# Kernel optimization log

Measured on AMD Instinct MI355X. Metric: run time of the kernel, lower is better.

The kernel has to match this reference:

```python
import jax, jax.numpy as jnp
import numpy as np

B, T, A_DIM, Z_DIM, K = 128, 80, 32, 64, 16


def setup_inputs() -> dict:
    key = jax.random.key(0)
    k1, k2, k3, k4 = jax.random.split(key, 4)
    obs = jax.random.normal(k1, (B, T, A_DIM), jnp.float32)
    alpha_logits = jax.random.normal(k2, (B, T, K), jnp.float32)
    # torch init: A = eye(z) repeated K times; small noise keeps 80-step recursion stable
    A_K = jnp.eye(Z_DIM, dtype=jnp.float32)[None] + 0.005 * jax.random.normal(k3, (K, Z_DIM, Z_DIM), jnp.float32)
    # torch init: C = 0.05 * randn
    C_K = 0.05 * jax.random.normal(k4, (K, A_DIM, Z_DIM), jnp.float32)
    return {"obs": obs, "alpha_logits": alpha_logits, "A_K": A_K, "C_K": C_K}


def _kalman(obs, A, C):
    # obs [B,T,a], A [B,T,z,z], C [B,T,a,z]
    Bq, Tq, a_dim = obs.shape
    z_dim = A.shape[-1]
    dt = obs.dtype
    Q = 0.08 * jnp.eye(z_dim, dtype=dt)
    R = 0.03 * jnp.eye(a_dim, dtype=dt)
    I = jnp.eye(z_dim, dtype=dt)

    obs_t = jnp.swapaxes(obs, 0, 1)          # [T,B,a]
    A_t = jnp.swapaxes(A, 0, 1)              # [T,B,z,z]
    C_t = jnp.swapaxes(C, 0, 1)              # [T,B,a,z]
    A_next = jnp.concatenate([A_t[1:], A_t[-1:]], axis=0)  # A[t+1]; last unused

    mu0 = jnp.zeros((Bq, z_dim), dt)
    sig0 = jnp.broadcast_to(20.0 * I, (Bq, z_dim, z_dim))

    def filt_step(carry, inp):
        mu_p, sig_p, mu_prev = carry
        At, Anx, Ct, y = inp
        CtT = jnp.swapaxes(Ct, -1, -2)
        S = Ct @ sig_p @ CtT + R                       # [B,a,a]
        Kg = sig_p @ CtT @ jnp.linalg.inv(S)            # [B,z,a]
        Amu = jnp.einsum('bij,bj->bi', At, mu_prev)     # A_t mu_{t-1}
        err = y - jnp.einsum('bij,bj->bi', Ct, Amu)
        mu_f = Amu + jnp.einsum('bij,bj->bi', Kg, err)
        sig_f = (I - Kg @ Ct) @ sig_p
        mu_pn = jnp.einsum('bij,bj->bi', Anx, mu_f)     # prediction with A_{t+1}
        sig_pn = Anx @ sig_f @ jnp.swapaxes(Anx, -1, -2) + Q
        return (mu_pn, sig_pn, mu_f), (mu_f, sig_f, mu_p, sig_p)

    _, (mu_f, sig_f, mu_p, sig_p) = jax.lax.scan(
        filt_step, (mu0, sig0, mu0), (A_t, A_next, C_t, obs_t))

    def smooth_step(carry, inp):
        mu_s, sig_s = carry
        mf, sf, Anx, mpn, spn = inp
        J = sf @ jnp.swapaxes(Anx, -1, -2) @ jnp.linalg.inv(spn)
        mu = mf + jnp.einsum('bij,bj->bi', J, mu_s - mpn)
        sig = sf + J @ (sig_s - spn) @ jnp.swapaxes(J, -1, -2)
        return (mu, sig), (mu, sig)

    init = (mu_f[-1], sig_f[-1])
    _, (mu_sm, sig_sm) = jax.lax.scan(
        smooth_step, init,
        (mu_f[:-1], sig_f[:-1], A_t[1:], mu_p[1:], sig_p[1:]),
        reverse=True)
    mu_sm = jnp.concatenate([mu_sm, mu_f[-1:]], axis=0)
    sig_sm = jnp.concatenate([sig_sm, sig_f[-1:]], axis=0)
    return jnp.swapaxes(mu_sm, 0, 1), jnp.swapaxes(sig_sm, 0, 1)  # [B,T,z], [B,T,z,z]


def reference(obs, alpha_logits, A_K, C_K):
    w = jax.nn.softmax(alpha_logits, axis=-1)                # [B,T,K]
    A = jnp.einsum('btk,kij->btij', w, A_K)                  # [B,T,z,z]
    C = jnp.einsum('btk,kij->btij', w, C_K)                  # [B,T,a,z]
    return _kalman(obs, A, C)
```

## Files before the change

### kernel.cpp

```cpp
#include <hip/hip_runtime.h>

#define B_ 128
#define T_ 80
#define AD 32
#define ZD 64
#define KD 16
#define S8 68
#define S4 34

template<int KL, int AS, int BS, bool ATRANS>
__device__ __forceinline__ void mm64(const float* __restrict__ Pa, const float* __restrict__ Qb,
                                     float acc[2][4], int r2, int c4)
{
#pragma unroll 8
    for (int k = 0; k < KL; k++) {
        float aA, aB;
        if (ATRANS) { aA = Pa[k * AS + r2];   aB = Pa[k * AS + r2 + 1]; }
        else        { aA = Pa[r2 * AS + k];   aB = Pa[(r2 + 1) * AS + k]; }
        const float4 bv = *(const float4*)&Qb[k * BS + c4];
        acc[0][0] += aA * bv.x; acc[0][1] += aA * bv.y; acc[0][2] += aA * bv.z; acc[0][3] += aA * bv.w;
        acc[1][0] += aB * bv.x; acc[1][1] += aB * bv.y; acc[1][2] += aB * bv.z; acc[1][3] += aB * bv.w;
    }
}

__global__ __launch_bounds__(512, 2)
void kvae_kernel(const float* __restrict__ obs, const float* __restrict__ logits,
                 const float* __restrict__ AK, const float* __restrict__ CK,
                 float* __restrict__ out)
{
    __shared__ __align__(16) float W[T_ * KD];
    __shared__ __align__(16) float Am[ZD * S8];
    __shared__ __align__(16) float At[ZD * S8];
    __shared__ __align__(16) float SP[ZD * S8];
    __shared__ __align__(16) float SF[ZD * S8];
    __shared__ __align__(16) float Mm[ZD * S8];
    __shared__ __align__(16) float Pool[9792];
    __shared__ __align__(16) float y_s[32];
    __shared__ __align__(16) float mup[64];
    __shared__ __align__(16) float muf[64];
    __shared__ __align__(16) float mus[64];
    __shared__ __align__(16) float mpn[64];
    __shared__ __align__(16) float dv[64];

    float* T1 = Pool;
    float* CM = Pool + 2176;
    float* CT = Pool + 4352;
    float* U_ = Pool + 6528;
    float* S_ = Pool + 8704;
    float* Xb = Pool;
    float* SG = Pool + 4352;

    const int tid = threadIdx.x;
    const int b   = blockIdx.x;

    const int r16 = tid >> 4;
    const int cg  = tid & 15;
    const int c4  = cg << 2;
    const int c2  = cg << 1;
    const int r2  = r16 << 1;
    const int i64 = tid >> 3;
    const int c8  = (tid & 7) << 3;

    const float* obs_b = obs    + (size_t)b * T_ * AD;
    const float* lg_b  = logits + (size_t)b * T_ * KD;
    float* omu = out + (size_t)b * T_ * ZD;
    float* osg = out + (size_t)B_ * T_ * ZD + (size_t)b * T_ * ZD * ZD;
    const float4* AK4 = (const float4*)AK;
    const float4* CK4 = (const float4*)CK;

    auto mixA_full = [&](int tt) {
#pragma unroll
        for (int rr = 0; rr < 2; rr++) {
            int r = r2 + rr;
            float4 a = make_float4(0.f, 0.f, 0.f, 0.f);
#pragma unroll
            for (int k = 0; k < KD; k++) {
                float wk = W[tt * KD + k];
                float4 v = AK4[k * 1024 + r * 16 + cg];
                a.x += wk * v.x; a.y += wk * v.y; a.z += wk * v.z; a.w += wk * v.w;
            }
            *(float4*)&Am[r * S8 + c4] = a;
            At[(c4 + 0) * S8 + r] = a.x; At[(c4 + 1) * S8 + r] = a.y;
            At[(c4 + 2) * S8 + r] = a.z; At[(c4 + 3) * S8 + r] = a.w;
        }
    };
    auto mixC_full = [&](int tt) {
        float4 a = make_float4(0.f, 0.f, 0.f, 0.f);
#pragma unroll
        for (int k = 0; k < KD; k++) {
            float wk = W[tt * KD + k];
            float4 v = CK4[k * 512 + r16 * 16 + cg];
            a.x += wk * v.x; a.y += wk * v.y; a.z += wk * v.z; a.w += wk * v.w;
        }
        *(float4*)&CM[r16 * S8 + c4] = a;
        CT[(c4 + 0) * S4 + r16] = a.x; CT[(c4 + 1) * S4 + r16] = a.y;
        CT[(c4 + 2) * S4 + r16] = a.z; CT[(c4 + 3) * S4 + r16] = a.w;
    };

    if (tid < T_) {
        float l[KD]; float mx = -1e30f;
#pragma unroll
        for (int k = 0; k < KD; k++) { l[k] = lg_b[tid * KD + k]; mx = fmaxf(mx, l[k]); }
        float s = 0.f;
#pragma unroll
        for (int k = 0; k < KD; k++) { l[k] = expf(l[k] - mx); s += l[k]; }
        float inv = 1.0f / s;
#pragma unroll
        for (int k = 0; k < KD; k++) W[tid * KD + k] = l[k] * inv;
    }
#pragma unroll
    for (int rr = 0; rr < 2; rr++) {
        int r = r2 + rr;
#pragma unroll
        for (int j = 0; j < 4; j++) SP[r * S8 + c4 + j] = (r == c4 + j) ? 20.0f : 0.0f;
    }
    if (tid < ZD) mup[tid] = 0.0f;
    __syncthreads();

    for (int t = 0; t < T_; t++) {
        if (t < T_ - 1) mixA_full(t + 1);
        mixC_full(t);
        if (tid < AD) y_s[tid] = obs_b[t * AD + tid];
        __syncthreads();

        {
            float a0 = 0, a1 = 0, a2 = 0, a3 = 0;
            const float* pa = CM + r16 * S8;
#pragma unroll 8
            for (int k = 0; k < ZD; k++) {
                float a = pa[k];
                float4 bv = *(const float4*)&SP[k * S8 + c4];
                a0 += a * bv.x; a1 += a * bv.y; a2 += a * bv.z; a3 += a * bv.w;
            }
            T1[r16 * S8 + c4 + 0] = a0; T1[r16 * S8 + c4 + 1] = a1;
            T1[r16 * S8 + c4 + 2] = a2; T1[r16 * S8 + c4 + 3] = a3;
        }
        __syncthreads();

        float4 ur; float ue = 0.f;
        {
            float a0 = 0, a1 = 0;
            const float* pa = T1 + r16 * S8;
#pragma unroll 8
            for (int k = 0; k < ZD; k++) {
                float a = pa[k];
                float2 bv = *(const float2*)&CT[k * S4 + c2];
                a0 += a * bv.x; a1 += a * bv.y;
            }
            if (r16 == c2)     a0 += 0.03f;
            if (r16 == c2 + 1) a1 += 0.03f;
            S_[r16 * S4 + c2] = a0; S_[r16 * S4 + c2 + 1] = a1;
            ur = *(const float4*)&T1[r16 * S8 + c4];
            if (cg == 15) {
                float s = 0.f;
                const float* pc = CM + r16 * S8;
#pragma unroll 8
                for (int k = 0; k < ZD; k++) s += pc[k] * mup[k];
                ue = y_s[r16] - s;
            }
            if (r16 < 2) {
                *(float4*)&U_[r16 * S8 + c4] = ur;
                if (cg == 15) U_[r16 * S8 + 64] = ue;
            }
        }
        __syncthreads();

#pragma unroll 1
        for (int j = 0; j < 16; j++) {
            const int p0 = 2 * j, p1 = p0 + 1;
            const int i = r16;
            const float f0 = S_[i * S4 + p0], f1 = S_[i * S4 + p1];
            const float qa = S_[p0 * S4 + p0], qb = S_[p0 * S4 + p1];
            const float qc = S_[p1 * S4 + p0], qd = S_[p1 * S4 + p1];
            const float l0x = S_[p0 * S4 + c2], l0y = S_[p0 * S4 + c2 + 1];
            const float l1x = S_[p1 * S4 + c2], l1y = S_[p1 * S4 + c2 + 1];
            const float4 r0 = *(const float4*)&U_[p0 * S8 + c4];
            const float4 r1 = *(const float4*)&U_[p1 * S8 + c4];
            float e0 = 0.f, e1 = 0.f;
            if (cg == 15) { e0 = U_[p0 * S8 + 64]; e1 = U_[p1 * S8 + 64]; }
            __syncthreads();
            const float dinv = 1.0f / (qa * qd - qb * qc);
            const float i00 =  qd * dinv, i01 = -qb * dinv;
            const float i10 = -qc * dinv, i11 =  qa * dinv;
            const float n0x = i00 * l0x + i01 * l1x, n0y = i00 * l0y + i01 * l1y;
            const float n1x = i10 * l0x + i11 * l1x, n1y = i10 * l0y + i11 * l1y;
            float4 m0, m1;
            m0.x = i00 * r0.x + i01 * r1.x; m0.y = i00 * r0.y + i01 * r1.y;
            m0.z = i00 * r0.z + i01 * r1.z; m0.w = i00 * r0.w + i01 * r1.w;
            m1.x = i10 * r0.x + i11 * r1.x; m1.y = i10 * r0.y + i11 * r1.y;
            m1.z = i10 * r0.z + i11 * r1.z; m1.w = i10 * r0.w + i11 * r1.w;
            const float me0 = i00 * e0 + i01 * e1, me1 = i10 * e0 + i11 * e1;
            if (i == p0) {
                S_[i * S4 + c2] = n0x; S_[i * S4 + c2 + 1] = n0y;
                ur = m0; if (cg == 15) ue = me0;
            } else if (i == p1) {
                S_[i * S4 + c2] = n1x; S_[i * S4 + c2 + 1] = n1y;
                ur = m1; if (cg == 15) ue = me1;
            } else {
                S_[i * S4 + c2]     -= f0 * n0x + f1 * n1x;
                S_[i * S4 + c2 + 1] -= f0 * n0y + f1 * n1y;
                ur.x -= f0 * m0.x + f1 * m1.x; ur.y -= f0 * m0.y + f1 * m1.y;
                ur.z -= f0 * m0.z + f1 * m1.z; ur.w -= f0 * m0.w + f1 * m1.w;
                if (cg == 15) ue -= f0 * me0 + f1 * me1;
            }
            if (j < 15 && (i == p0 + 2 || i == p0 + 3)) {
                *(float4*)&U_[i * S8 + c4] = ur;
                if (cg == 15) U_[i * S8 + 64] = ue;
            }
            __syncthreads();
        }
        *(float4*)&U_[r16 * S8 + c4] = ur;
        if (cg == 15) U_[r16 * S8 + 64] = ue;
        __syncthreads();

        {
            float acc[2][4] = {};
            mm64<AD, S8, S8, true>(T1, U_, acc, r2, c4);
            float* og = osg + (size_t)t * ZD * ZD;
#pragma unroll
            for (int rr = 0; rr < 2; rr++) {
                int r = r2 + rr;
                float4 sp = *(const float4*)&SP[r * S8 + c4];
                float4 v;
                v.x = sp.x - acc[rr][0]; v.y = sp.y - acc[rr][1];
                v.z = sp.z - acc[rr][2]; v.w = sp.w - acc[rr][3];
                *(float4*)&SF[r * S8 + c4] = v;
                *(float4*)(og + r * ZD + c4) = v;
            }
        }
        if (tid < ZD) {
            float s = 0.f;
#pragma unroll
            for (int k = 0; k < AD; k++) s += T1[k * S8 + tid] * U_[k * S8 + 64];
            float v = mup[tid] + s;
            muf[tid] = v;
            omu[t * ZD + tid] = v;
        }
        __syncthreads();

        if (t < T_ - 1) {
            {
                float acc[2][4] = {};
                mm64<ZD, S8, S8, false>(Am, SF, acc, r2, c4);
#pragma unroll
                for (int rr = 0; rr < 2; rr++)
                    *(float4*)&Mm[(r2 + rr) * S8 + c4] =
                        make_float4(acc[rr][0], acc[rr][1], acc[rr][2], acc[rr][3]);
            }
            __syncthreads();
            {
                float acc[2][4] = {};
                mm64<ZD, S8, S8, false>(Mm, At, acc, r2, c4);
#pragma unroll
                for (int rr = 0; rr < 2; rr++) {
                    int r = r2 + rr;
#pragma unroll
                    for (int j = 0; j < 4; j++)
                        SP[r * S8 + c4 + j] = acc[rr][j] + ((r == c4 + j) ? 0.08f : 0.0f);
                }
            }
            if (tid >= 448) {
                int i = tid - 448;
                float s = 0.f;
                const float* pa = Am + i * S8;
#pragma unroll 8
                for (int k = 0; k < ZD; k++) s += pa[k] * muf[k];
                mup[i] = s;
            }
            __syncthreads();
        }
    }

#pragma unroll
    for (int rr = 0; rr < 2; rr++) {
        int r = r2 + rr;
        *(float4*)&SG[r * S8 + c4] = *(const float4*)&SF[r * S8 + c4];
    }
    if (tid < ZD) mus[tid] = muf[tid];
    __syncthreads();

    for (int t = T_ - 2; t >= 0; t--) {
        mixA_full(t + 1);
        {
            const float4* og4 = (const float4*)(osg + (size_t)t * ZD * ZD);
#pragma unroll
            for (int rr = 0; rr < 2; rr++) {
                int r = r2 + rr;
                *(float4*)&SF[r * S8 + c4] = og4[r * 16 + cg];
            }
        }
        if (tid >= 448) muf[tid - 448] = omu[t * ZD + (tid - 448)];
        __syncthreads();

        {
            float acc[2][4] = {};
            mm64<ZD, S8, S8, false>(Am, SF, acc, r2, c4);
#pragma unroll
            for (int rr = 0; rr < 2; rr++) {
                int r = r2 + rr;
                float4 v = make_float4(acc[rr][0], acc[rr][1], acc[rr][2], acc[rr][3]);
                *(float4*)&Mm[r * S8 + c4] = v;
                *(float4*)&Xb[r * S8 + c4] = v;
            }
        }
        if (tid >= 448) {
            int i = tid - 448;
            float s = 0.f;
            const float* pa = Am + i * S8;
#pragma unroll 8
            for (int k = 0; k < ZD; k++) s += pa[k] * muf[k];
            mpn[i] = s;
        }
        __syncthreads();

        {
            float acc[2][4] = {};
            mm64<ZD, S8, S8, false>(Mm, At, acc, r2, c4);
#pragma unroll
            for (int rr = 0; rr < 2; rr++) {
                int r = r2 + rr;
#pragma unroll
                for (int j = 0; j < 4; j++)
                    SP[r * S8 + c4 + j] = acc[rr][j] + ((r == c4 + j) ? 0.08f : 0.0f);
            }
        }
        if (tid >= 448) { int i = tid - 448; dv[i] = mus[i] - mpn[i]; }
        __syncthreads();

        float4 xr0 = *(const float4*)&Xb[i64 * S8 + c8];
        float4 xr1 = *(const float4*)&Xb[i64 * S8 + c8 + 4];
#pragma unroll 1
        for (int j = 0; j < 32; j++) {
            const int p0 = 2 * j, p1 = p0 + 1;
            const float f0 = SP[i64 * S8 + p0], f1 = SP[i64 * S8 + p1];
            const float qa = SP[p0 * S8 + p0], qb = SP[p0 * S8 + p1];
            const float qc = SP[p1 * S8 + p0], qd = SP[p1 * S8 + p1];
            const float4 l0a = *(const float4*)&SP[p0 * S8 + c8];
            const float4 l0b = *(const float4*)&SP[p0 * S8 + c8 + 4];
            const float4 l1a = *(const float4*)&SP[p1 * S8 + c8];
            const float4 l1b = *(const float4*)&SP[p1 * S8 + c8 + 4];
            const float4 r0a = *(const float4*)&Xb[p0 * S8 + c8];
            const float4 r0b = *(const float4*)&Xb[p0 * S8 + c8 + 4];
            const float4 r1a = *(const float4*)&Xb[p1 * S8 + c8];
            const float4 r1b = *(const float4*)&Xb[p1 * S8 + c8 + 4];
            const float4 ol0 = *(const float4*)&SP[i64 * S8 + c8];
            const float4 ol1 = *(const float4*)&SP[i64 * S8 + c8 + 4];
            __syncthreads();
            const float dinv = 1.0f / (qa * qd - qb * qc);
            const float i00 =  qd * dinv, i01 = -qb * dinv;
            const float i10 = -qc * dinv, i11 =  qa * dinv;
            float4 nl0a, nl0b, nl1a, nl1b, nr0a, nr0b, nr1a, nr1b;
            nl0a.x = i00*l0a.x + i01*l1a.x; nl0a.y = i00*l0a.y + i01*l1a.y;
            nl0a.z = i00*l0a.z + i01*l1a.z; nl0a.w = i00*l0a.w + i01*l1a.w;
            nl0b.x = i00*l0b.x + i01*l1b.x; nl0b.y = i00*l0b.y + i01*l1b.y;
            nl0b.z = i00*l0b.z + i01*l1b.z; nl0b.w = i00*l0b.w + i01*l1b.w;
            nl1a.x = i10*l0a.x + i11*l1a.x; nl1a.y = i10*l0a.y + i11*l1a.y;
            nl1a.z = i10*l0a.z + i11*l1a.z; nl1a.w = i10*l0a.w + i11*l1a.w;
            nl1b.x = i10*l0b.x + i11*l1b.x; nl1b.y = i10*l0b.y + i11*l1b.y;
            nl1b.z = i10*l0b.z + i11*l1b.z; nl1b.w = i10*l0b.w + i11*l1b.w;
            nr0a.x = i00*r0a.x + i01*r1a.x; nr0a.y = i00*r0a.y + i01*r1a.y;
            nr0a.z = i00*r0a.z + i01*r1a.z; nr0a.w = i00*r0a.w + i01*r1a.w;
            nr0b.x = i00*r0b.x + i01*r1b.x; nr0b.y = i00*r0b.y + i01*r1b.y;
            nr0b.z = i00*r0b.z + i01*r1b.z; nr0b.w = i00*r0b.w + i01*r1b.w;
            nr1a.x = i10*r0a.x + i11*r1a.x; nr1a.y = i10*r0a.y + i11*r1a.y;
            nr1a.z = i10*r0a.z + i11*r1a.z; nr1a.w = i10*r0a.w + i11*r1a.w;
            nr1b.x = i10*r0b.x + i11*r1b.x; nr1b.y = i10*r0b.y + i11*r1b.y;
            nr1b.z = i10*r0b.z + i11*r1b.z; nr1b.w = i10*r0b.w + i11*r1b.w;
            if (i64 == p0) {
                *(float4*)&SP[i64 * S8 + c8]     = nl0a;
                *(float4*)&SP[i64 * S8 + c8 + 4] = nl0b;
                xr0 = nr0a; xr1 = nr0b;
            } else if (i64 == p1) {
                *(float4*)&SP[i64 * S8 + c8]     = nl1a;
                *(float4*)&SP[i64 * S8 + c8 + 4] = nl1b;
                xr0 = nr1a; xr1 = nr1b;
            } else {
                float4 w0 = ol0, w1 = ol1;
                w0.x -= f0*nl0a.x + f1*nl1a.x; w0.y -= f0*nl0a.y + f1*nl1a.y;
                w0.z -= f0*nl0a.z + f1*nl1a.z; w0.w -= f0*nl0a.w + f1*nl1a.w;
                w1.x -= f0*nl0b.x + f1*nl1b.x; w1.y -= f0*nl0b.y + f1*nl1b.y;
                w1.z -= f0*nl0b.z + f1*nl1b.z; w1.w -= f0*nl0b.w + f1*nl1b.w;
                *(float4*)&SP[i64 * S8 + c8]     = w0;
                *(float4*)&SP[i64 * S8 + c8 + 4] = w1;
                xr0.x -= f0*nr0a.x + f1*nr1a.x; xr0.y -= f0*nr0a.y + f1*nr1a.y;
                xr0.z -= f0*nr0a.z + f1*nr1a.z; xr0.w -= f0*nr0a.w + f1*nr1a.w;
                xr1.x -= f0*nr0b.x + f1*nr1b.x; xr1.y -= f0*nr0b.y + f1*nr1b.y;
                xr1.z -= f0*nr0b.z + f1*nr1b.z; xr1.w -= f0*nr0b.w + f1*nr1b.w;
            }
            if (j < 31 && (i64 == p0 + 2 || i64 == p0 + 3)) {
                *(float4*)&Xb[i64 * S8 + c8]     = xr0;
                *(float4*)&Xb[i64 * S8 + c8 + 4] = xr1;
            }
            __syncthreads();
        }
        *(float4*)&Xb[i64 * S8 + c8]     = xr0;
        *(float4*)&Xb[i64 * S8 + c8 + 4] = xr1;
        __syncthreads();

        {
            float acc[2][4] = {};
            mm64<ZD, S8, S8, false>(SG, Xb, acc, r2, c4);
#pragma unroll
            for (int rr = 0; rr < 2; rr++) {
                int r = r2 + rr;
                float4 m = *(const float4*)&Mm[r * S8 + c4];
                SP[r * S8 + c4 + 0] = acc[rr][0] - m.x;
                SP[r * S8 + c4 + 1] = acc[rr][1] - m.y;
                SP[r * S8 + c4 + 2] = acc[rr][2] - m.z;
                SP[r * S8 + c4 + 3] = acc[rr][3] - m.w;
            }
        }
        __syncthreads();

        {
            float acc[2][4] = {};
            mm64<ZD, S8, S8, true>(Xb, SP, acc, r2, c4);
            float* og = osg + (size_t)t * ZD * ZD;
#pragma unroll
            for (int rr = 0; rr < 2; rr++) {
                int r = r2 + rr;
                float4 sf = *(const float4*)&SF[r * S8 + c4];
                float4 v;
                v.x = sf.x + acc[rr][0]; v.y = sf.y + acc[rr][1];
                v.z = sf.z + acc[rr][2]; v.w = sf.w + acc[rr][3];
                *(float4*)&SG[r * S8 + c4] = v;
                *(float4*)(og + r * ZD + c4) = v;
            }
        }
        if (tid < ZD) {
            float s = 0.f;
#pragma unroll 8
            for (int k = 0; k < ZD; k++) s += Xb[k * S8 + tid] * dv[k];
            float v = muf[tid] + s;
            mus[tid] = v;
            omu[t * ZD + tid] = v;
        }
        __syncthreads();
    }
}

extern "C" void kernel_launch(void* const* d_in, const int* in_sizes, int n_in,
                              void* d_out, int out_size, void* d_ws, size_t ws_size,
                              hipStream_t stream) {
    const float* obs = (const float*)d_in[0];
    const float* lg  = (const float*)d_in[1];
    const float* AK  = (const float*)d_in[2];
    const float* CK  = (const float*)d_in[3];
    (void)d_ws; (void)ws_size; (void)in_sizes; (void)n_in; (void)out_size;
    kvae_kernel<<<dim3(B_), dim3(512), 0, stream>>>(obs, lg, AK, CK, (float*)d_out);
}
```

Baseline: 3.979 ms.

## Rewrite Kalman kernel with 256 threads, 4x4 register tiles and pivot-broadcast elimination

Halves the block to 256 threads and gives each thread a 4x4 output tile in the 64x64 matrix products, with both operands read as float4. The Gauss-Jordan solves keep their rows in registers and publish only the next pivot rows and factors into double-buffered shared arrays, so the per-step serial solve work and shared traffic shrink. The symmetric predicted covariance is built for the upper triangle only and then mirrored. The cost is more registers per thread and a larger, more intricate kernel that is harder to check.

```diff
diff --git a/kernel.cpp b/kernel.cpp
--- a/kernel.cpp
+++ b/kernel.cpp
@@ -5,37 +5,54 @@
 #define AD 32
 #define ZD 64
 #define KD 16
-#define S8 68
-#define S4 34
-
-template<int KL, int AS, int BS, bool ATRANS>
-__device__ __forceinline__ void mm64(const float* __restrict__ Pa, const float* __restrict__ Qb,
-                                     float acc[2][4], int r2, int c4)
+#define SZ 68
+#define SC 36
+
+__device__ __forceinline__ float4 ld4(const float* p) { return *(const float4*)p; }
+__device__ __forceinline__ void st4f(float* p, float4 v) { *(float4*)p = v; }
+__device__ __forceinline__ float4 comb2(float a, float4 x, float b, float4 y) {
+    return make_float4(a*x.x + b*y.x, a*x.y + b*y.y, a*x.z + b*y.z, a*x.w + b*y.w);
+}
+__device__ __forceinline__ float4 elim2(float4 c, float g0, float4 x, float g1, float4 y) {
+    c.x -= g0*x.x + g1*y.x; c.y -= g0*x.y + g1*y.y;
+    c.z -= g0*x.z + g1*y.z; c.w -= g0*x.w + g1*y.w;
+    return c;
+}
+
+template<int KL, int AS, int BS>
+__device__ __forceinline__ void mmT44(const float* __restrict__ PaT, const float* __restrict__ Qb,
+                                      float acc[4][4], int r4, int c4)
 {
 #pragma unroll 8
-    for (int k = 0; k < KL; k++) {
-        float aA, aB;
-        if (ATRANS) { aA = Pa[k * AS + r2];   aB = Pa[k * AS + r2 + 1]; }
-        else        { aA = Pa[r2 * AS + k];   aB = Pa[(r2 + 1) * AS + k]; }
-        const float4 bv = *(const float4*)&Qb[k * BS + c4];
-        acc[0][0] += aA * bv.x; acc[0][1] += aA * bv.y; acc[0][2] += aA * bv.z; acc[0][3] += aA * bv.w;
-        acc[1][0] += aB * bv.x; acc[1][1] += aB * bv.y; acc[1][2] += aB * bv.z; acc[1][3] += aB * bv.w;
+    for (int k = 0; k < KL; ++k) {
+        const float4 av = ld4(&PaT[k*AS + r4]);
+        const float4 bv = ld4(&Qb[k*BS + c4]);
+        acc[0][0] += av.x*bv.x; acc[0][1] += av.x*bv.y; acc[0][2] += av.x*bv.z; acc[0][3] += av.x*bv.w;
+        acc[1][0] += av.y*bv.x; acc[1][1] += av.y*bv.y; acc[1][2] += av.y*bv.z; acc[1][3] += av.y*bv.w;
+        acc[2][0] += av.z*bv.x; acc[2][1] += av.z*bv.y; acc[2][2] += av.z*bv.z; acc[2][3] += av.z*bv.w;
+        acc[3][0] += av.w*bv.x; acc[3][1] += av.w*bv.y; acc[3][2] += av.w*bv.z; acc[3][3] += av.w*bv.w;
     }
 }
 
-__global__ __launch_bounds__(512, 2)
+__global__ __launch_bounds__(256, 1)
 void kvae_kernel(const float* __restrict__ obs, const float* __restrict__ logits,
                  const float* __restrict__ AK, const float* __restrict__ CK,
                  float* __restrict__ out)
 {
     __shared__ __align__(16) float W[T_ * KD];
-    __shared__ __align__(16) float Am[ZD * S8];
-    __shared__ __align__(16) float At[ZD * S8];
-    __shared__ __align__(16) float SP[ZD * S8];
-    __shared__ __align__(16) float SF[ZD * S8];
-    __shared__ __align__(16) float Mm[ZD * S8];
-    __shared__ __align__(16) float Pool[9792];
+    __shared__ __align__(16) float Am[ZD * SZ];
+    __shared__ __align__(16) float At[ZD * SZ];
+    __shared__ __align__(16) float SP[ZD * SZ];
+    __shared__ __align__(16) float SF[ZD * SZ];
+    __shared__ __align__(16) float MT[ZD * SZ];
+    __shared__ __align__(16) float Pool[9984];
+    __shared__ __align__(16) float pvL[256];
+    __shared__ __align__(16) float pvR[256];
+    __shared__ __align__(16) float fb[256];
+    __shared__ __align__(16) float pvE[4];
     __shared__ __align__(16) float y_s[32];
+    __shared__ __align__(16) float errv[32];
+    __shared__ __align__(16) float uev[32];
     __shared__ __align__(16) float mup[64];
     __shared__ __align__(16) float muf[64];
     __shared__ __align__(16) float mus[64];
@@ -45,21 +62,22 @@
     float* T1 = Pool;
     float* CM = Pool + 2176;
     float* CT = Pool + 4352;
-    float* U_ = Pool + 6528;
-    float* S_ = Pool + 8704;
-    float* Xb = Pool;
-    float* SG = Pool + 4352;
+    float* S_ = Pool + 6656;
+    float* U_ = Pool + 7808;
+    float* SG = Pool;
+    float* Xb = Pool + 4352;
 
     const int tid = threadIdx.x;
     const int b   = blockIdx.x;
-
-    const int r16 = tid >> 4;
     const int cg  = tid & 15;
     const int c4  = cg << 2;
+    const int r4  = (tid >> 4) << 2;
+    const int r2  = (tid >> 4) << 1;
     const int c2  = cg << 1;
-    const int r2  = r16 << 1;
-    const int i64 = tid >> 3;
-    const int c8  = (tid & 7) << 3;
+    const int gi  = tid >> 2;
+    const int gs  = tid & 3;
+    const int hi  = tid >> 3;
+    const int hs  = tid & 7;
 
     const float* obs_b = obs    + (size_t)b * T_ * AD;
     const float* lg_b  = logits + (size_t)b * T_ * KD;
@@ -68,33 +86,37 @@
     const float4* AK4 = (const float4*)AK;
     const float4* CK4 = (const float4*)CK;
 
-    auto mixA_full = [&](int tt) {
-#pragma unroll
-        for (int rr = 0; rr < 2; rr++) {
-            int r = r2 + rr;
+    auto mixA = [&](int tt) {
+#pragma unroll
+        for (int q = 0; q < 4; q++) {
+            const int r = r4 + q;
             float4 a = make_float4(0.f, 0.f, 0.f, 0.f);
 #pragma unroll
             for (int k = 0; k < KD; k++) {
-                float wk = W[tt * KD + k];
-                float4 v = AK4[k * 1024 + r * 16 + cg];
+                const float wk = W[tt * KD + k];
+                const float4 v = AK4[k * 1024 + r * 16 + cg];
                 a.x += wk * v.x; a.y += wk * v.y; a.z += wk * v.z; a.w += wk * v.w;
             }
-            *(float4*)&Am[r * S8 + c4] = a;
-            At[(c4 + 0) * S8 + r] = a.x; At[(c4 + 1) * S8 + r] = a.y;
-            At[(c4 + 2) * S8 + r] = a.z; At[(c4 + 3) * S8 + r] = a.w;
+            st4f(&Am[r * SZ + c4], a);
+            At[(c4 + 0) * SZ + r] = a.x; At[(c4 + 1) * SZ + r] = a.y;
+            At[(c4 + 2) * SZ + r] = a.z; At[(c4 + 3) * SZ + r] = a.w;
         }
     };
-    auto mixC_full = [&](int tt) {
-        float4 a = make_float4(0.f, 0.f, 0.f, 0.f);
-#pragma unroll
-        for (int k = 0; k < KD; k++) {
-            float wk = W[tt * KD + k];
-            float4 v = CK4[k * 512 + r16 * 16 + cg];
-            a.x += wk * v.x; a.y += wk * v.y; a.z += wk * v.z; a.w += wk * v.w;
-        }
-        *(float4*)&CM[r16 * S8 + c4] = a;
-        CT[(c4 + 0) * S4 + r16] = a.x; CT[(c4 + 1) * S4 + r16] = a.y;
-        CT[(c4 + 2) * S4 + r16] = a.z; CT[(c4 + 3) * S4 + r16] = a.w;
+    auto mixC = [&](int tt) {
+#pragma unroll
+        for (int q = 0; q < 2; q++) {
+            const int r = r2 + q;
+            float4 a = make_float4(0.f, 0.f, 0.f, 0.f);
+#pragma unroll
+            for (int k = 0; k < KD; k++) {
+                const float wk = W[tt * KD + k];
+                const float4 v = CK4[k * 512 + r * 16 + cg];
+                a.x += wk * v.x; a.y += wk * v.y; a.z += wk * v.z; a.w += wk * v.w;
+            }
+            st4f(&CM[r * SZ + c4], a);
+            CT[(c4 + 0) * SC + r] = a.x; CT[(c4 + 1) * SC + r] = a.y;
+            CT[(c4 + 2) * SC + r] = a.z; CT[(c4 + 3) * SC + r] = a.w;
+        }
     };
 
     if (tid < T_) {
@@ -104,135 +126,189 @@
         float s = 0.f;
 #pragma unroll
         for (int k = 0; k < KD; k++) { l[k] = expf(l[k] - mx); s += l[k]; }
-        float inv = 1.0f / s;
+        const float inv = 1.0f / s;
 #pragma unroll
         for (int k = 0; k < KD; k++) W[tid * KD + k] = l[k] * inv;
     }
 #pragma unroll
-    for (int rr = 0; rr < 2; rr++) {
-        int r = r2 + rr;
-#pragma unroll
-        for (int j = 0; j < 4; j++) SP[r * S8 + c4 + j] = (r == c4 + j) ? 20.0f : 0.0f;
+    for (int q = 0; q < 4; q++) {
+        const int r = r4 + q;
+#pragma unroll
+        for (int j = 0; j < 4; j++) SP[r * SZ + c4 + j] = (r == c4 + j) ? 20.0f : 0.0f;
     }
     if (tid < ZD) mup[tid] = 0.0f;
     __syncthreads();
 
     for (int t = 0; t < T_; t++) {
-        if (t < T_ - 1) mixA_full(t + 1);
-        mixC_full(t);
+        if (t < T_ - 1) mixA(t + 1);
+        mixC(t);
         if (tid < AD) y_s[tid] = obs_b[t * AD + tid];
         __syncthreads();
 
         {
-            float a0 = 0, a1 = 0, a2 = 0, a3 = 0;
-            const float* pa = CM + r16 * S8;
+            float a0[4] = {0,0,0,0}, a1[4] = {0,0,0,0};
 #pragma unroll 8
-            for (int k = 0; k < ZD; k++) {
-                float a = pa[k];
-                float4 bv = *(const float4*)&SP[k * S8 + c4];
-                a0 += a * bv.x; a1 += a * bv.y; a2 += a * bv.z; a3 += a * bv.w;
-            }
-            T1[r16 * S8 + c4 + 0] = a0; T1[r16 * S8 + c4 + 1] = a1;
-            T1[r16 * S8 + c4 + 2] = a2; T1[r16 * S8 + c4 + 3] = a3;
-        }
-        __syncthreads();
-
-        float4 ur; float ue = 0.f;
-        {
-            float a0 = 0, a1 = 0;
-            const float* pa = T1 + r16 * S8;
-#pragma unroll 8
-            for (int k = 0; k < ZD; k++) {
-                float a = pa[k];
-                float2 bv = *(const float2*)&CT[k * S4 + c2];
-                a0 += a * bv.x; a1 += a * bv.y;
-            }
-            if (r16 == c2)     a0 += 0.03f;
-            if (r16 == c2 + 1) a1 += 0.03f;
-            S_[r16 * S4 + c2] = a0; S_[r16 * S4 + c2 + 1] = a1;
-            ur = *(const float4*)&T1[r16 * S8 + c4];
-            if (cg == 15) {
-                float s = 0.f;
-                const float* pc = CM + r16 * S8;
-#pragma unroll 8
-                for (int k = 0; k < ZD; k++) s += pc[k] * mup[k];
-                ue = y_s[r16] - s;
-            }
-            if (r16 < 2) {
-                *(float4*)&U_[r16 * S8 + c4] = ur;
-                if (cg == 15) U_[r16 * S8 + 64] = ue;
-            }
-        }
-        __syncthreads();
+            for (int k = 0; k < ZD; ++k) {
+                const float2 av = *(const float2*)&CT[k * SC + r2];
+                const float4 bv = ld4(&SP[k * SZ + c4]);
+                a0[0] += av.x*bv.x; a0[1] += av.x*bv.y; a0[2] += av.x*bv.z; a0[3] += av.x*bv.w;
+                a1[0] += av.y*bv.x; a1[1] += av.y*bv.y; a1[2] += av.y*bv.z; a1[3] += av.y*bv.w;
+            }
+            st4f(&T1[r2 * SZ + c4], make_float4(a0[0], a0[1], a0[2], a0[3]));
+            st4f(&T1[(r2 + 1) * SZ + c4], make_float4(a1[0], a1[1], a1[2], a1[3]));
+        }
+        __syncthreads();
+
+        {
+            float s00 = 0, s01 = 0, s10 = 0, s11 = 0;
+#pragma unroll 4
+            for (int k4 = 0; k4 < ZD; k4 += 4) {
+                const float4 t0 = ld4(&T1[r2 * SZ + k4]);
+                const float4 t1 = ld4(&T1[(r2 + 1) * SZ + k4]);
+                const float4 u0 = ld4(&CM[c2 * SZ + k4]);
+                const float4 u1 = ld4(&CM[(c2 + 1) * SZ + k4]);
+                s00 += t0.x*u0.x + t0.y*u0.y + t0.z*u0.z + t0.w*u0.w;
+                s01 += t0.x*u1.x + t0.y*u1.y + t0.z*u1.z + t0.w*u1.w;
+                s10 += t1.x*u0.x + t1.y*u0.y + t1.z*u0.z + t1.w*u0.w;
+                s11 += t1.x*u1.x + t1.y*u1.y + t1.z*u1.z + t1.w*u1.w;
+            }
+            if (r2 == c2) { s00 += 0.03f; s11 += 0.03f; }
+            if (r2 + 1 == c2) s10 += 0.03f;
+            if (c2 + 1 == r2) s01 += 0.03f;
+            S_[r2 * SC + c2] = s00;       S_[r2 * SC + c2 + 1] = s01;
+            S_[(r2 + 1) * SC + c2] = s10; S_[(r2 + 1) * SC + c2 + 1] = s11;
+        }
+        if (tid < AD) {
+            float s = 0.f;
+#pragma unroll
+            for (int k4 = 0; k4 < ZD; k4 += 4) {
+                const float4 cm = ld4(&CM[tid * SZ + k4]);
+                const float4 mu = ld4(&mup[k4]);
+                s += cm.x*mu.x + cm.y*mu.y + cm.z*mu.z + cm.w*mu.w;
+            }
+            errv[tid] = y_s[tid] - s;
+        }
+        __syncthreads();
+
+        {
+            float4 aL0, aL1, aL2, aL3, aR0, aR1, aR2, aR3; float ge = 0.f;
+            aL0 = aL1 = aL2 = aL3 = aR0 = aR1 = aR2 = aR3 = make_float4(0, 0, 0, 0);
+            if (hs < 2) {
+                const float* p = &S_[hi * SC + hs * 16];
+                aL0 = ld4(p); aL1 = ld4(p + 4); aL2 = ld4(p + 8); aL3 = ld4(p + 12);
+            } else if (hs < 6) {
+                const float* p = &T1[hi * SZ + (hs - 2) * 16];
+                aR0 = ld4(p); aR1 = ld4(p + 4); aR2 = ld4(p + 8); aR3 = ld4(p + 12);
+            } else if (hs == 6) ge = errv[hi];
+            if (hi < 2) {
+                if (hs < 2) {
+                    float* q = &pvL[hi * 64 + hs * 16];
+                    st4f(q, aL0); st4f(q + 4, aL1); st4f(q + 8, aL2); st4f(q + 12, aL3);
+                } else if (hs < 6) {
+                    float* q = &pvR[hi * 64 + (hs - 2) * 16];
+                    st4f(q, aR0); st4f(q + 4, aR1); st4f(q + 8, aR2); st4f(q + 12, aR3);
+                } else if (hs == 6) pvE[hi] = ge;
+            }
+            if (hs == 0) { fb[hi * 2] = aL0.x; fb[hi * 2 + 1] = aL0.y; }
+            __syncthreads();
 
 #pragma unroll 1
-        for (int j = 0; j < 16; j++) {
-            const int p0 = 2 * j, p1 = p0 + 1;
-            const int i = r16;
-            const float f0 = S_[i * S4 + p0], f1 = S_[i * S4 + p1];
-            const float qa = S_[p0 * S4 + p0], qb = S_[p0 * S4 + p1];
-            const float qc = S_[p1 * S4 + p0], qd = S_[p1 * S4 + p1];
-            const float l0x = S_[p0 * S4 + c2], l0y = S_[p0 * S4 + c2 + 1];
-            const float l1x = S_[p1 * S4 + c2], l1y = S_[p1 * S4 + c2 + 1];
-            const float4 r0 = *(const float4*)&U_[p0 * S8 + c4];
-            const float4 r1 = *(const float4*)&U_[p1 * S8 + c4];
-            float e0 = 0.f, e1 = 0.f;
-            if (cg == 15) { e0 = U_[p0 * S8 + 64]; e1 = U_[p1 * S8 + 64]; }
-            __syncthreads();
-            const float dinv = 1.0f / (qa * qd - qb * qc);
-            const float i00 =  qd * dinv, i01 = -qb * dinv;
-            const float i10 = -qc * dinv, i11 =  qa * dinv;
-            const float n0x = i00 * l0x + i01 * l1x, n0y = i00 * l0y + i01 * l1y;
-            const float n1x = i10 * l0x + i11 * l1x, n1y = i10 * l0y + i11 * l1y;
-            float4 m0, m1;
-            m0.x = i00 * r0.x + i01 * r1.x; m0.y = i00 * r0.y + i01 * r1.y;
-            m0.z = i00 * r0.z + i01 * r1.z; m0.w = i00 * r0.w + i01 * r1.w;
-            m1.x = i10 * r0.x + i11 * r1.x; m1.y = i10 * r0.y + i11 * r1.y;
-            m1.z = i10 * r0.z + i11 * r1.z; m1.w = i10 * r0.w + i11 * r1.w;
-            const float me0 = i00 * e0 + i01 * e1, me1 = i10 * e0 + i11 * e1;
-            if (i == p0) {
-                S_[i * S4 + c2] = n0x; S_[i * S4 + c2 + 1] = n0y;
-                ur = m0; if (cg == 15) ue = me0;
-            } else if (i == p1) {
-                S_[i * S4 + c2] = n1x; S_[i * S4 + c2 + 1] = n1y;
-                ur = m1; if (cg == 15) ue = me1;
-            } else {
-                S_[i * S4 + c2]     -= f0 * n0x + f1 * n1x;
-                S_[i * S4 + c2 + 1] -= f0 * n0y + f1 * n1y;
-                ur.x -= f0 * m0.x + f1 * m1.x; ur.y -= f0 * m0.y + f1 * m1.y;
-                ur.z -= f0 * m0.z + f1 * m1.z; ur.w -= f0 * m0.w + f1 * m1.w;
-                if (cg == 15) ue -= f0 * me0 + f1 * me1;
-            }
-            if (j < 15 && (i == p0 + 2 || i == p0 + 3)) {
-                *(float4*)&U_[i * S8 + c4] = ur;
-                if (cg == 15) U_[i * S8 + 64] = ue;
-            }
-            __syncthreads();
-        }
-        *(float4*)&U_[r16 * S8 + c4] = ur;
-        if (cg == 15) U_[r16 * S8 + 64] = ue;
-        __syncthreads();
-
-        {
-            float acc[2][4] = {};
-            mm64<AD, S8, S8, true>(T1, U_, acc, r2, c4);
+            for (int j8 = 0; j8 < 2; ++j8) {
+#pragma unroll
+                for (int jj = 0; jj < 8; ++jj) {
+                    const int j = j8 * 8 + jj;
+                    const int par = j & 1, nb = par ^ 1;
+                    const int p0 = 2 * j, p1 = p0 + 1;
+                    const float qa = pvL[par * 128 + p0],      qbv = pvL[par * 128 + p1];
+                    const float qc = pvL[par * 128 + 64 + p0], qd  = pvL[par * 128 + 64 + p1];
+                    const float f0 = fb[par * 128 + hi * 2], f1 = fb[par * 128 + hi * 2 + 1];
+                    const float dinv = 1.0f / (qa * qd - qbv * qc);
+                    const float i00 = qd * dinv, i01 = -qbv * dinv, i10 = -qc * dinv, i11 = qa * dinv;
+                    const float g0 = f0 * i00 + f1 * i10;
+                    const float g1 = f0 * i01 + f1 * i11;
+                    if (hs < 2) {
+                        const float* pl0 = &pvL[par * 128 + hs * 16];
+                        const float* pl1 = &pvL[par * 128 + 64 + hs * 16];
+                        const float4 x0 = ld4(pl0), x1 = ld4(pl0 + 4), x2 = ld4(pl0 + 8), x3 = ld4(pl0 + 12);
+                        const float4 z0 = ld4(pl1), z1 = ld4(pl1 + 4), z2 = ld4(pl1 + 8), z3 = ld4(pl1 + 12);
+                        if (hi == p0) {
+                            aL0 = comb2(i00, x0, i01, z0); aL1 = comb2(i00, x1, i01, z1);
+                            aL2 = comb2(i00, x2, i01, z2); aL3 = comb2(i00, x3, i01, z3);
+                        } else if (hi == p1) {
+                            aL0 = comb2(i10, x0, i11, z0); aL1 = comb2(i10, x1, i11, z1);
+                            aL2 = comb2(i10, x2, i11, z2); aL3 = comb2(i10, x3, i11, z3);
+                        } else {
+                            aL0 = elim2(aL0, g0, x0, g1, z0); aL1 = elim2(aL1, g0, x1, g1, z1);
+                            aL2 = elim2(aL2, g0, x2, g1, z2); aL3 = elim2(aL3, g0, x3, g1, z3);
+                        }
+                        if (j < 15 && (hi == p0 + 2 || hi == p0 + 3)) {
+                            float* q = &pvL[nb * 128 + (hi & 1) * 64 + hs * 16];
+                            st4f(q, aL0); st4f(q + 4, aL1); st4f(q + 8, aL2); st4f(q + 12, aL3);
+                        }
+                    } else if (hs < 6) {
+                        const float* pr0 = &pvR[par * 128 + (hs - 2) * 16];
+                        const float* pr1 = &pvR[par * 128 + 64 + (hs - 2) * 16];
+                        const float4 x0 = ld4(pr0), x1 = ld4(pr0 + 4), x2 = ld4(pr0 + 8), x3 = ld4(pr0 + 12);
+                        const float4 z0 = ld4(pr1), z1 = ld4(pr1 + 4), z2 = ld4(pr1 + 8), z3 = ld4(pr1 + 12);
+                        if (hi == p0) {
+                            aR0 = comb2(i00, x0, i01, z0); aR1 = comb2(i00, x1, i01, z1);
+                            aR2 = comb2(i00, x2, i01, z2); aR3 = comb2(i00, x3, i01, z3);
+                        } else if (hi == p1) {
+                            aR0 = comb2(i10, x0, i11, z0); aR1 = comb2(i10, x1, i11, z1);
+                            aR2 = comb2(i10, x2, i11, z2); aR3 = comb2(i10, x3, i11, z3);
+                        } else {
+                            aR0 = elim2(aR0, g0, x0, g1, z0); aR1 = elim2(aR1, g0, x1, g1, z1);
+                            aR2 = elim2(aR2, g0, x2, g1, z2); aR3 = elim2(aR3, g0, x3, g1, z3);
+                        }
+                        if (j < 15 && (hi == p0 + 2 || hi == p0 + 3)) {
+                            float* q = &pvR[nb * 128 + (hi & 1) * 64 + (hs - 2) * 16];
+                            st4f(q, aR0); st4f(q + 4, aR1); st4f(q + 8, aR2); st4f(q + 12, aR3);
+                        }
+                    } else if (hs == 6) {
+                        const float e0 = pvE[par * 2], e1 = pvE[par * 2 + 1];
+                        const float me0 = i00 * e0 + i01 * e1, me1 = i10 * e0 + i11 * e1;
+                        if (hi == p0) ge = me0;
+                        else if (hi == p1) ge = me1;
+                        else ge -= f0 * me0 + f1 * me1;
+                        if (j < 15 && (hi == p0 + 2 || hi == p0 + 3)) pvE[nb * 2 + (hi & 1)] = ge;
+                    }
+                    if (j < 15 && hs == ((j + 1) >> 3)) {
+                        const int pc = (2 * jj + 2) & 15;
+                        const float v0 = (pc==0)?aL0.x:(pc==2)?aL0.z:(pc==4)?aL1.x:(pc==6)?aL1.z:
+                                         (pc==8)?aL2.x:(pc==10)?aL2.z:(pc==12)?aL3.x:aL3.z;
+                        const float v1 = (pc==0)?aL0.y:(pc==2)?aL0.w:(pc==4)?aL1.y:(pc==6)?aL1.w:
+                                         (pc==8)?aL2.y:(pc==10)?aL2.w:(pc==12)?aL3.y:aL3.w;
+                        fb[nb * 128 + hi * 2] = v0; fb[nb * 128 + hi * 2 + 1] = v1;
+                    }
+                    __syncthreads();
+                }
+            }
+            if (hs >= 2 && hs < 6) {
+                float* q = &U_[hi * SZ + (hs - 2) * 16];
+                st4f(q, aR0); st4f(q + 4, aR1); st4f(q + 8, aR2); st4f(q + 12, aR3);
+            } else if (hs == 6) uev[hi] = ge;
+        }
+        __syncthreads();
+
+        {
+            float acc[4][4] = {};
+            mmT44<AD, SZ, SZ>(T1, U_, acc, r4, c4);
             float* og = osg + (size_t)t * ZD * ZD;
 #pragma unroll
-            for (int rr = 0; rr < 2; rr++) {
-                int r = r2 + rr;
-                float4 sp = *(const float4*)&SP[r * S8 + c4];
-                float4 v;
-                v.x = sp.x - acc[rr][0]; v.y = sp.y - acc[rr][1];
-                v.z = sp.z - acc[rr][2]; v.w = sp.w - acc[rr][3];
-                *(float4*)&SF[r * S8 + c4] = v;
+            for (int q = 0; q < 4; q++) {
+                const int r = r4 + q;
+                const float4 sp = ld4(&SP[r * SZ + c4]);
+                const float4 v = make_float4(sp.x - acc[q][0], sp.y - acc[q][1],
+                                             sp.z - acc[q][2], sp.w - acc[q][3]);
+                st4f(&SF[r * SZ + c4], v);
                 *(float4*)(og + r * ZD + c4) = v;
             }
         }
         if (tid < ZD) {
             float s = 0.f;
 #pragma unroll
-            for (int k = 0; k < AD; k++) s += T1[k * S8 + tid] * U_[k * S8 + 64];
-            float v = mup[tid] + s;
+            for (int k = 0; k < AD; k++) s += T1[k * SZ + tid] * uev[k];
+            const float v = mup[tid] + s;
             muf[tid] = v;
             omu[t * ZD + tid] = v;
         }
@@ -240,198 +316,232 @@
 
         if (t < T_ - 1) {
             {
-                float acc[2][4] = {};
-                mm64<ZD, S8, S8, false>(Am, SF, acc, r2, c4);
-#pragma unroll
-                for (int rr = 0; rr < 2; rr++)
-                    *(float4*)&Mm[(r2 + rr) * S8 + c4] =
-                        make_float4(acc[rr][0], acc[rr][1], acc[rr][2], acc[rr][3]);
+                float acc[4][4] = {};
+                mmT44<ZD, SZ, SZ>(SF, At, acc, r4, c4);
+#pragma unroll
+                for (int q = 0; q < 4; q++)
+                    st4f(&MT[(r4 + q) * SZ + c4],
+                         make_float4(acc[q][0], acc[q][1], acc[q][2], acc[q][3]));
             }
             __syncthreads();
-            {
-                float acc[2][4] = {};
-                mm64<ZD, S8, S8, false>(Mm, At, acc, r2, c4);
-#pragma unroll
-                for (int rr = 0; rr < 2; rr++) {
-                    int r = r2 + rr;
+            if (r4 <= c4) {
+                float acc[4][4] = {};
+                mmT44<ZD, SZ, SZ>(MT, At, acc, r4, c4);
+#pragma unroll
+                for (int q = 0; q < 4; q++) {
+                    const int r = r4 + q;
 #pragma unroll
                     for (int j = 0; j < 4; j++)
-                        SP[r * S8 + c4 + j] = acc[rr][j] + ((r == c4 + j) ? 0.08f : 0.0f);
+                        SP[r * SZ + c4 + j] = acc[q][j] + ((r == c4 + j) ? 0.08f : 0.0f);
                 }
             }
-            if (tid >= 448) {
-                int i = tid - 448;
+            __syncthreads();
+            if (r4 > c4) {
+                float4 m0 = ld4(&SP[(c4 + 0) * SZ + r4]);
+                float4 m1 = ld4(&SP[(c4 + 1) * SZ + r4]);
+                float4 m2 = ld4(&SP[(c4 + 2) * SZ + r4]);
+                float4 m3 = ld4(&SP[(c4 + 3) * SZ + r4]);
+                st4f(&SP[(r4 + 0) * SZ + c4], make_float4(m0.x, m1.x, m2.x, m3.x));
+                st4f(&SP[(r4 + 1) * SZ + c4], make_float4(m0.y, m1.y, m2.y, m3.y));
+                st4f(&SP[(r4 + 2) * SZ + c4], make_float4(m0.z, m1.z, m2.z, m3.z));
+                st4f(&SP[(r4 + 3) * SZ + c4], make_float4(m0.w, m1.w, m2.w, m3.w));
+            }
+            if (tid < ZD) {
                 float s = 0.f;
-                const float* pa = Am + i * S8;
-#pragma unroll 8
-                for (int k = 0; k < ZD; k++) s += pa[k] * muf[k];
-                mup[i] = s;
+#pragma unroll
+                for (int k4 = 0; k4 < ZD; k4 += 4) {
+                    const float4 am = ld4(&Am[tid * SZ + k4]);
+                    const float4 mf = ld4(&muf[k4]);
+                    s += am.x*mf.x + am.y*mf.y + am.z*mf.z + am.w*mf.w;
+                }
+                mup[tid] = s;
             }
             __syncthreads();
         }
     }
 
 #pragma unroll
-    for (int rr = 0; rr < 2; rr++) {
-        int r = r2 + rr;
-        *(float4*)&SG[r * S8 + c4] = *(const float4*)&SF[r * S8 + c4];
-    }
+    for (int q = 0; q < 4; q++)
+        st4f(&SG[(r4 + q) * SZ + c4], ld4(&SF[(r4 + q) * SZ + c4]));
     if (tid < ZD) mus[tid] = muf[tid];
     __syncthreads();
 
     for (int t = T_ - 2; t >= 0; t--) {
-        mixA_full(t + 1);
-        {
-            const float4* og4 = (const float4*)(osg + (size_t)t * ZD * ZD);
-#pragma unroll
-            for (int rr = 0; rr < 2; rr++) {
-                int r = r2 + rr;
-                *(float4*)&SF[r * S8 + c4] = og4[r * 16 + cg];
-            }
-        }
-        if (tid >= 448) muf[tid - 448] = omu[t * ZD + (tid - 448)];
-        __syncthreads();
-
-        {
-            float acc[2][4] = {};
-            mm64<ZD, S8, S8, false>(Am, SF, acc, r2, c4);
-#pragma unroll
-            for (int rr = 0; rr < 2; rr++) {
-                int r = r2 + rr;
-                float4 v = make_float4(acc[rr][0], acc[rr][1], acc[rr][2], acc[rr][3]);
-                *(float4*)&Mm[r * S8 + c4] = v;
-                *(float4*)&Xb[r * S8 + c4] = v;
-            }
-        }
-        if (tid >= 448) {
-            int i = tid - 448;
-            float s = 0.f;
-            const float* pa = Am + i * S8;
-#pragma unroll 8
-            for (int k = 0; k < ZD; k++) s += pa[k] * muf[k];
-            mpn[i] = s;
-        }
-        __syncthreads();
-
-        {
-            float acc[2][4] = {};
-            mm64<ZD, S8, S8, false>(Mm, At, acc, r2, c4);
-#pragma unroll
-            for (int rr = 0; rr < 2; rr++) {
-                int r = r2 + rr;
-#pragma unroll
-                for (int j = 0; j < 4; j++)
-                    SP[r * S8 + c4 + j] = acc[rr][j] + ((r == c4 + j) ? 0.08f : 0.0f);
-            }
-        }
-        if (tid >= 448) { int i = tid - 448; dv[i] = mus[i] - mpn[i]; }
-        __syncthreads();
-
-        float4 xr0 = *(const float4*)&Xb[i64 * S8 + c8];
-        float4 xr1 = *(const float4*)&Xb[i64 * S8 + c8 + 4];
-#pragma unroll 1
-        for (int j = 0; j < 32; j++) {
-            const int p0 = 2 * j, p1 = p0 + 1;
-            const float f0 = SP[i64 * S8 + p0], f1 = SP[i64 * S8 + p1];
-            const float qa = SP[p0 * S8 + p0], qb = SP[p0 * S8 + p1];
-            const float qc = SP[p1 * S8 + p0], qd = SP[p1 * S8 + p1];
-            const float4 l0a = *(const float4*)&SP[p0 * S8 + c8];
-            const float4 l0b = *(const float4*)&SP[p0 * S8 + c8 + 4];
-            const float4 l1a = *(const float4*)&SP[p1 * S8 + c8];
-            const float4 l1b = *(const float4*)&SP[p1 * S8 + c8 + 4];
-            const float4 r0a = *(const float4*)&Xb[p0 * S8 + c8];
-            const float4 r0b = *(const float4*)&Xb[p0 * S8 + c8 + 4];
-            const float4 r1a = *(const float4*)&Xb[p1 * S8 + c8];
-            const float4 r1b = *(const float4*)&Xb[p1 * S8 + c8 + 4];
-            const float4 ol0 = *(const float4*)&SP[i64 * S8 + c8];
-            const float4 ol1 = *(const float4*)&SP[i64 * S8 + c8 + 4];
-            __syncthreads();
-            const float dinv = 1.0f / (qa * qd - qb * qc);
-            const float i00 =  qd * dinv, i01 = -qb * dinv;
-            const float i10 = -qc * dinv, i11 =  qa * dinv;
-            float4 nl0a, nl0b, nl1a, nl1b, nr0a, nr0b, nr1a, nr1b;
-            nl0a.x = i00*l0a.x + i01*l1a.x; nl0a.y = i00*l0a.y + i01*l1a.y;
-            nl0a.z = i00*l0a.z + i01*l1a.z; nl0a.w = i00*l0a.w + i01*l1a.w;
-            nl0b.x = i00*l0b.x + i01*l1b.x; nl0b.y = i00*l0b.y + i01*l1b.y;
-            nl0b.z = i00*l0b.z + i01*l1b.z; nl0b.w = i00*l0b.w + i01*l1b.w;
-            nl1a.x = i10*l0a.x + i11*l1a.x; nl1a.y = i10*l0a.y + i11*l1a.y;
-            nl1a.z = i10*l0a.z + i11*l1a.z; nl1a.w = i10*l0a.w + i11*l1a.w;
-            nl1b.x = i10*l0b.x + i11*l1b.x; nl1b.y = i10*l0b.y + i11*l1b.y;
-            nl1b.z = i10*l0b.z + i11*l1b.z; nl1b.w = i10*l0b.w + i11*l1b.w;
-            nr0a.x = i00*r0a.x + i01*r1a.x; nr0a.y = i00*r0a.y + i01*r1a.y;
-            nr0a.z = i00*r0a.z + i01*r1a.z; nr0a.w = i00*r0a.w + i01*r1a.w;
-            nr0b.x = i00*r0b.x + i01*r1b.x; nr0b.y = i00*r0b.y + i01*r1b.y;
-            nr0b.z = i00*r0b.z + i01*r1b.z; nr0b.w = i00*r0b.w + i01*r1b.w;
-            nr1a.x = i10*r0a.x + i11*r1a.x; nr1a.y = i10*r0a.y + i11*r1a.y;
-            nr1a.z = i10*r0a.z + i11*r1a.z; nr1a.w = i10*r0a.w + i11*r1a.w;
-            nr1b.x = i10*r0b.x + i11*r1b.x; nr1b.y = i10*r0b.y + i11*r1b.y;
-            nr1b.z = i10*r0b.z + i11*r1b.z; nr1b.w = i10*r0b.w + i11*r1b.w;
-            if (i64 == p0) {
-                *(float4*)&SP[i64 * S8 + c8]     = nl0a;
-                *(float4*)&SP[i64 * S8 + c8 + 4] = nl0b;
-                xr0 = nr0a; xr1 = nr0b;
-            } else if (i64 == p1) {
-                *(float4*)&SP[i64 * S8 + c8]     = nl1a;
-                *(float4*)&SP[i64 * S8 + c8 + 4] = nl1b;
-                xr0 = nr1a; xr1 = nr1b;
-            } else {
-                float4 w0 = ol0, w1 = ol1;
-                w0.x -= f0*nl0a.x + f1*nl1a.x; w0.y -= f0*nl0a.y + f1*nl1a.y;
-                w0.z -= f0*nl0a.z + f1*nl1a.z; w0.w -= f0*nl0a.w + f1*nl1a.w;
-                w1.x -= f0*nl0b.x + f1*nl1b.x; w1.y -= f0*nl0b.y + f1*nl1b.y;
-                w1.z -= f0*nl0b.z + f1*nl1b.z; w1.w -= f0*nl0b.w + f1*nl1b.w;
-                *(float4*)&SP[i64 * S8 + c8]     = w0;
-                *(float4*)&SP[i64 * S8 + c8 + 4] = w1;
-                xr0.x -= f0*nr0a.x + f1*nr1a.x; xr0.y -= f0*nr0a.y + f1*nr1a.y;
-                xr0.z -= f0*nr0a.z + f1*nr1a.z; xr0.w -= f0*nr0a.w + f1*nr1a.w;
-                xr1.x -= f0*nr0b.x + f1*nr1b.x; xr1.y -= f0*nr0b.y + f1*nr1b.y;
-                xr1.z -= f0*nr0b.z + f1*nr1b.z; xr1.w -= f0*nr0b.w + f1*nr1b.w;
-            }
-            if (j < 31 && (i64 == p0 + 2 || i64 == p0 + 3)) {
-                *(float4*)&Xb[i64 * S8 + c8]     = xr0;
-                *(float4*)&Xb[i64 * S8 + c8 + 4] = xr1;
-            }
-            __syncthreads();
-        }
-        *(float4*)&Xb[i64 * S8 + c8]     = xr0;
-        *(float4*)&Xb[i64 * S8 + c8 + 4] = xr1;
-        __syncthreads();
-
-        {
-            float acc[2][4] = {};
-            mm64<ZD, S8, S8, false>(SG, Xb, acc, r2, c4);
-#pragma unroll
-            for (int rr = 0; rr < 2; rr++) {
-                int r = r2 + rr;
-                float4 m = *(const float4*)&Mm[r * S8 + c4];
-                SP[r * S8 + c4 + 0] = acc[rr][0] - m.x;
-                SP[r * S8 + c4 + 1] = acc[rr][1] - m.y;
-                SP[r * S8 + c4 + 2] = acc[rr][2] - m.z;
-                SP[r * S8 + c4 + 3] = acc[rr][3] - m.w;
-            }
-        }
-        __syncthreads();
-
-        {
-            float acc[2][4] = {};
-            mm64<ZD, S8, S8, true>(Xb, SP, acc, r2, c4);
-            float* og = osg + (size_t)t * ZD * ZD;
-#pragma unroll
-            for (int rr = 0; rr < 2; rr++) {
-                int r = r2 + rr;
-                float4 sf = *(const float4*)&SF[r * S8 + c4];
-                float4 v;
-                v.x = sf.x + acc[rr][0]; v.y = sf.y + acc[rr][1];
-                v.z = sf.z + acc[rr][2]; v.w = sf.w + acc[rr][3];
-                *(float4*)&SG[r * S8 + c4] = v;
-                *(float4*)(og + r * ZD + c4) = v;
-            }
+        mixA(t + 1);
+        {
+            const float* og = osg + (size_t)t * ZD * ZD;
+#pragma unroll
+            for (int q = 0; q < 4; q++)
+                st4f(&SF[(r4 + q) * SZ + c4], *(const float4*)(og + (r4 + q) * ZD + c4));
+        }
+        if (tid < ZD) muf[tid] = omu[t * ZD + tid];
+        __syncthreads();
+
+        {
+            float acc[4][4] = {};
+            mmT44<ZD, SZ, SZ>(SF, At, acc, r4, c4);
+#pragma unroll
+            for (int q = 0; q < 4; q++)
+                st4f(&MT[(r4 + q) * SZ + c4],
+                     make_float4(acc[q][0], acc[q][1], acc[q][2], acc[q][3]));
         }
         if (tid < ZD) {
             float s = 0.f;
-#pragma unroll 8
-            for (int k = 0; k < ZD; k++) s += Xb[k * S8 + tid] * dv[k];
-            float v = muf[tid] + s;
+#pragma unroll
+            for (int k4 = 0; k4 < ZD; k4 += 4) {
+                const float4 am = ld4(&Am[tid * SZ + k4]);
+                const float4 mf = ld4(&muf[k4]);
+                s += am.x*mf.x + am.y*mf.y + am.z*mf.z + am.w*mf.w;
+            }
+            mpn[tid] = s;
+        }
+        __syncthreads();
+
+        if (r4 <= c4) {
+            float acc[4][4] = {};
+            mmT44<ZD, SZ, SZ>(MT, At, acc, r4, c4);
+#pragma unroll
+            for (int q = 0; q < 4; q++) {
+                const int r = r4 + q;
+#pragma unroll
+                for (int j = 0; j < 4; j++)
+                    SP[r * SZ + c4 + j] = acc[q][j] + ((r == c4 + j) ? 0.08f : 0.0f);
+            }
+        }
+        __syncthreads();
+        if (r4 > c4) {
+            float4 m0 = ld4(&SP[(c4 + 0) * SZ + r4]);
+            float4 m1 = ld4(&SP[(c4 + 1) * SZ + r4]);
+            float4 m2 = ld4(&SP[(c4 + 2) * SZ + r4]);
+            float4 m3 = ld4(&SP[(c4 + 3) * SZ + r4]);
+            st4f(&SP[(r4 + 0) * SZ + c4], make_float4(m0.x, m1.x, m2.x, m3.x));
+            st4f(&SP[(r4 + 1) * SZ + c4], make_float4(m0.y, m1.y, m2.y, m3.y));
+            st4f(&SP[(r4 + 2) * SZ + c4], make_float4(m0.z, m1.z, m2.z, m3.z));
+            st4f(&SP[(r4 + 3) * SZ + c4], make_float4(m0.w, m1.w, m2.w, m3.w));
+        }
+        if (tid < ZD) dv[tid] = mus[tid] - mpn[tid];
+        __syncthreads();
+
+        {
+            float4 aL0, aL1, aL2, aL3, aR0, aR1, aR2, aR3;
+            {
+                const float* p = &SP[gi * SZ + gs * 16];
+                aL0 = ld4(p); aL1 = ld4(p + 4); aL2 = ld4(p + 8); aL3 = ld4(p + 12);
+                const int cb = gs * 16;
+                aR0 = make_float4(MT[(cb+0)*SZ+gi], MT[(cb+1)*SZ+gi], MT[(cb+2)*SZ+gi], MT[(cb+3)*SZ+gi]);
+                aR1 = make_float4(MT[(cb+4)*SZ+gi], MT[(cb+5)*SZ+gi], MT[(cb+6)*SZ+gi], MT[(cb+7)*SZ+gi]);
+                aR2 = make_float4(MT[(cb+8)*SZ+gi], MT[(cb+9)*SZ+gi], MT[(cb+10)*SZ+gi], MT[(cb+11)*SZ+gi]);
+                aR3 = make_float4(MT[(cb+12)*SZ+gi], MT[(cb+13)*SZ+gi], MT[(cb+14)*SZ+gi], MT[(cb+15)*SZ+gi]);
+                if (gi < 2) {
+                    float* q = &pvL[gi * 64 + gs * 16];
+                    st4f(q, aL0); st4f(q + 4, aL1); st4f(q + 8, aL2); st4f(q + 12, aL3);
+                    float* q2 = &pvR[gi * 64 + gs * 16];
+                    st4f(q2, aR0); st4f(q2 + 4, aR1); st4f(q2 + 8, aR2); st4f(q2 + 12, aR3);
+                }
+                if (gs == 0) { fb[gi * 2] = aL0.x; fb[gi * 2 + 1] = aL0.y; }
+            }
+            __syncthreads();
+
+#pragma unroll 1
+            for (int j8 = 0; j8 < 4; ++j8) {
+#pragma unroll
+                for (int jj = 0; jj < 8; ++jj) {
+                    const int j = j8 * 8 + jj;
+                    const int par = j & 1, nb = par ^ 1;
+                    const int p0 = 2 * j, p1 = p0 + 1;
+                    const float qa = pvL[par * 128 + p0],      qbv = pvL[par * 128 + p1];
+                    const float qc = pvL[par * 128 + 64 + p0], qd  = pvL[par * 128 + 64 + p1];
+                    const float f0 = fb[par * 128 + gi * 2], f1 = fb[par * 128 + gi * 2 + 1];
+                    const float dinv = 1.0f / (qa * qd - qbv * qc);
+                    const float i00 = qd * dinv, i01 = -qbv * dinv, i10 = -qc * dinv, i11 = qa * dinv;
+                    const float g0 = f0 * i00 + f1 * i10;
+                    const float g1 = f0 * i01 + f1 * i11;
+                    const float* pl0 = &pvL[par * 128 + gs * 16];
+                    const float* pl1 = &pvL[par * 128 + 64 + gs * 16];
+                    const float* pr0 = &pvR[par * 128 + gs * 16];
+                    const float* pr1 = &pvR[par * 128 + 64 + gs * 16];
+                    const float4 x0 = ld4(pl0), x1 = ld4(pl0 + 4), x2 = ld4(pl0 + 8), x3 = ld4(pl0 + 12);
+                    const float4 z0 = ld4(pl1), z1 = ld4(pl1 + 4), z2 = ld4(pl1 + 8), z3 = ld4(pl1 + 12);
+                    const float4 u0 = ld4(pr0), u1 = ld4(pr0 + 4), u2 = ld4(pr0 + 8), u3 = ld4(pr0 + 12);
+                    const float4 w0 = ld4(pr1), w1 = ld4(pr1 + 4), w2 = ld4(pr1 + 8), w3 = ld4(pr1 + 12);
+                    if (gi == p0) {
+                        aL0 = comb2(i00, x0, i01, z0); aL1 = comb2(i00, x1, i01, z1);
+                        aL2 = comb2(i00, x2, i01, z2); aL3 = comb2(i00, x3, i01, z3);
+                        aR0 = comb2(i00, u0, i01, w0); aR1 = comb2(i00, u1, i01, w1);
+                        aR2 = comb2(i00, u2, i01, w2); aR3 = comb2(i00, u3, i01, w3);
+                    } else if (gi == p1) {
+                        aL0 = comb2(i10, x0, i11, z0); aL1 = comb2(i10, x1, i11, z1);
+                        aL2 = comb2(i10, x2, i11, z2); aL3 = comb2(i10, x3, i11, z3);
+                        aR0 = comb2(i10, u0, i11, w0); aR1 = comb2(i10, u1, i11, w1);
+                        aR2 = comb2(i10, u2, i11, w2); aR3 = comb2(i10, u3, i11, w3);
+                    } else {
+                        aL0 = elim2(aL0, g0, x0, g1, z0); aL1 = elim2(aL1, g0, x1, g1, z1);
+                        aL2 = elim2(aL2, g0, x2, g1, z2); aL3 = elim2(aL3, g0, x3, g1, z3);
+                        aR0 = elim2(aR0, g0, u0, g1, w0); aR1 = elim2(aR1, g0, u1, g1, w1);
+                        aR2 = elim2(aR2, g0, u2, g1, w2); aR3 = elim2(aR3, g0, u3, g1, w3);
+                    }
+                    if (j < 31 && (gi == p0 + 2 || gi == p0 + 3)) {
+                        float* q = &pvL[nb * 128 + (gi & 1) * 64 + gs * 16];
+                        st4f(q, aL0); st4f(q + 4, aL1); st4f(q + 8, aL2); st4f(q + 12, aL3);
+                        float* q2 = &pvR[nb * 128 + (gi & 1) * 64 + gs * 16];
+                        st4f(q2, aR0); st4f(q2 + 4, aR1); st4f(q2 + 8, aR2); st4f(q2 + 12, aR3);
+                    }
+                    if (j < 31 && gs == ((j + 1) >> 3)) {
+                        const int pc = (2 * jj + 2) & 15;
+                        const float v0 = (pc==0)?aL0.x:(pc==2)?aL0.z:(pc==4)?aL1.x:(pc==6)?aL1.z:
+                                         (pc==8)?aL2.x:(pc==10)?aL2.z:(pc==12)?aL3.x:aL3.z;
+                        const float v1 = (pc==0)?aL0.y:(pc==2)?aL0.w:(pc==4)?aL1.y:(pc==6)?aL1.w:
+                                         (pc==8)?aL2.y:(pc==10)?aL2.w:(pc==12)?aL3.y:aL3.w;
+                        fb[nb * 128 + gi * 2] = v0; fb[nb * 128 + gi * 2 + 1] = v1;
+                    }
+                    __syncthreads();
+                }
+            }
+            {
+                float* q = &Xb[gi * SZ + gs * 16];
+                st4f(q, aR0); st4f(q + 4, aR1); st4f(q + 8, aR2); st4f(q + 12, aR3);
+            }
+        }
+        __syncthreads();
+
+        {
+            float acc[4][4] = {};
+            mmT44<ZD, SZ, SZ>(SG, Xb, acc, r4, c4);
+            const float4 m0 = ld4(&MT[(c4 + 0) * SZ + r4]);
+            const float4 m1 = ld4(&MT[(c4 + 1) * SZ + r4]);
+            const float4 m2 = ld4(&MT[(c4 + 2) * SZ + r4]);
+            const float4 m3 = ld4(&MT[(c4 + 3) * SZ + r4]);
+            acc[0][0] -= m0.x; acc[0][1] -= m1.x; acc[0][2] -= m2.x; acc[0][3] -= m3.x;
+            acc[1][0] -= m0.y; acc[1][1] -= m1.y; acc[1][2] -= m2.y; acc[1][3] -= m3.y;
+            acc[2][0] -= m0.z; acc[2][1] -= m1.z; acc[2][2] -= m2.z; acc[2][3] -= m3.z;
+            acc[3][0] -= m0.w; acc[3][1] -= m1.w; acc[3][2] -= m2.w; acc[3][3] -= m3.w;
+            __syncthreads();
+#pragma unroll
+            for (int q = 0; q < 4; q++)
+                st4f(&SP[(r4 + q) * SZ + c4],
+                     make_float4(acc[q][0], acc[q][1], acc[q][2], acc[q][3]));
+        }
+        __syncthreads();
+
+        {
+            float acc[4][4] = {};
+            mmT44<ZD, SZ, SZ>(Xb, SP, acc, r4, c4);
+            float* og = osg + (size_t)t * ZD * ZD;
+#pragma unroll
+            for (int q = 0; q < 4; q++) {
+                const int r = r4 + q;
+                const float4 sf = ld4(&SF[r * SZ + c4]);
+                const float4 v = make_float4(sf.x + acc[q][0], sf.y + acc[q][1],
+                                             sf.z + acc[q][2], sf.w + acc[q][3]);
+                st4f(&SG[r * SZ + c4], v);
+                *(float4*)(og + r * ZD + c4) = v;
+            }
+        }
+        if (tid < ZD) {
+            float s = 0.f;
+#pragma unroll
+            for (int k = 0; k < ZD; k++) s += Xb[k * SZ + tid] * dv[k];
+            const float v = muf[tid] + s;
             mus[tid] = v;
             omu[t * ZD + tid] = v;
         }
@@ -447,5 +557,5 @@
     const float* AK  = (const float*)d_in[2];
     const float* CK  = (const float*)d_in[3];
     (void)d_ws; (void)ws_size; (void)in_sizes; (void)n_in; (void)out_size;
-    kvae_kernel<<<dim3(B_), dim3(512), 0, stream>>>(obs, lg, AK, CK, (float*)d_out);
+    kvae_kernel<<<dim3(B_), dim3(256), 0, stream>>>(obs, lg, AK, CK, (float*)d_out);
 }
```

Result: slower. 5.877 ms (+47.7%).
